# Optimization experiments

Hardware: AMD Instinct MI355X
Metric: run time of the kernel (lower is better)

## Reference

```python
import jax, jax.numpy as jnp
import numpy as np

B, T, Q, H = 128, 50, 1024, 256
MAX_STEP = 50
TEMP = 0.5
SUP_W, DIST_W, EMBED_W, LOSS_WEIGHT = 1.0, 0.01, 1.0, 1.0
BLUR, DIAMETER, REACH, SCALING, P = 0.005, 1.0, 500.0, 0.5, 2
NEG = -1e9


def _softmin(eps, C, h):
    # h: log-weights + potential/eps over the second axis of C
    return -eps * jax.nn.logsumexp(h[None, :] - C / eps, axis=1)


def _sqcost(u, v):
    sq = jnp.sum(u * u, -1)[:, None] + jnp.sum(v * v, -1)[None, :] - 2.0 * (u @ v.T)
    return 0.5 * jnp.maximum(sq, 0.0)  # geomloss p=2 cost: |x-y|^2 / 2


def sinkhorn_divergence(x, y):
    # geomloss SamplesLoss('sinkhorn', p=2, blur=0.005, diameter=1, reach=500),
    # tensorized, debiased, unbalanced, eps-scaling schedule.
    N, M = x.shape[0], y.shape[0]
    a_log = jnp.full((N,), -np.log(float(N)), dtype=x.dtype)
    b_log = jnp.full((M,), -np.log(float(M)), dtype=x.dtype)
    Cxy, Cyx = _sqcost(x, y), _sqcost(y, x)
    Cxx, Cyy = _sqcost(x, x), _sqcost(y, y)
    rho = REACH ** P
    eps_final = BLUR ** P
    eps_list = []
    e = DIAMETER ** P
    while e > eps_final:
        eps_list.append(e)
        e = e * (SCALING ** P)
    eps_list.append(eps_final)
    f_ab = jnp.zeros((N,), x.dtype)
    g_ab = jnp.zeros((M,), x.dtype)
    f_aa = jnp.zeros((N,), x.dtype)
    g_bb = jnp.zeros((M,), x.dtype)
    for eps in eps_list:  # static schedule (~9 steps)
        damp = 1.0 / (1.0 + eps / rho)
        ft = damp * _softmin(eps, Cxy, b_log + g_ab / eps)
        gt = damp * _softmin(eps, Cyx, a_log + f_ab / eps)
        faa = 0.5 * (f_aa + damp * _softmin(eps, Cxx, a_log + f_aa / eps))
        gbb = 0.5 * (g_bb + damp * _softmin(eps, Cyy, b_log + g_bb / eps))
        f_ab, g_ab, f_aa, g_bb = ft, gt, faa, gbb
    w = rho + eps_final / 2.0  # UnbalancedWeight
    a_w, b_w = jnp.exp(a_log), jnp.exp(b_log)
    return (jnp.sum(a_w * w * (jnp.exp(-f_aa / rho) - jnp.exp(-f_ab / rho)))
            + jnp.sum(b_w * w * (jnp.exp(-g_bb / rho) - jnp.exp(-g_ab / rho))))


def _forward(lc, lt, le, ltc, ltt, lte, ohs, oht, ods, odt, batch):
    p_c, p_t, p_e = lc / TEMP, lt / TEMP, le / TEMP
    q_c, q_t, q_e = ltc / TEMP, ltt / TEMP, lte / TEMP
    flat = lambda z: z.reshape(z.shape[0], -1)
    loss_kd = (sinkhorn_divergence(flat(p_c), flat(q_c))
               + sinkhorn_divergence(flat(p_t), flat(q_t))
               + sinkhorn_divergence(flat(p_e), flat(q_e)))
    S = MAX_STEP - 1
    delta = batch[:, :, :Q] + batch[:, :, Q:]  # [B,T,Q] question one-hots
    a = jnp.floor(((batch[:, :, :Q] - batch[:, :, Q:]).sum(-1) + 1.0) / 2.0)[:, 1:1 + S]  # [B,S] correctness
    dsh = delta[:, 1:1 + S]  # [B,S,Q]
    # diagonal of p[:S] @ delta[1:].T == per-step gather of next question's logit
    pc = jnp.einsum('bsq,bsq->bs', p_c[:, :S], dsh)
    pt = jnp.einsum('bsq,bsq->bs', p_t[:, :S], dsh)
    pe = jnp.einsum('bsq,bsq->bs', p_e[:, :S], dsh)
    idx = jnp.arange(S)
    last = jnp.max(jnp.where(pc > 0, idx[None, :], -1), axis=1)  # last i with pc[i] > 0
    L = jnp.where(last >= 0, last + 1, S)  # no break => keep full length
    mask = idx[None, :] < L[:, None]
    def ce(logits):
        m = jnp.where(mask, logits, NEG)
        lsm = m - jax.nn.logsumexp(m, axis=1, keepdims=True)
        return -jnp.sum(jnp.where(mask, a * lsm, 0.0))  # soft-target CE, summed over students
    loss_sup = ce(pt) + ce(pc) + ce(pe)
    embed = 0.5 * (jnp.sum((ohs - oht) ** 2) + jnp.sum((ods - odt) ** 2))
    total = LOSS_WEIGHT * (SUP_W * loss_sup + DIST_W * loss_kd + EMBED_W * embed)
    return total.reshape(1)


def setup_inputs():
    key = jax.random.key(0)
    ks = jax.random.split(key, 12)
    rn = lambda k, s: jax.random.normal(k, s, dtype=jnp.float32)
    qid = jax.random.randint(ks[10], (B, T), 0, Q)
    correct = jax.random.randint(ks[11], (B, T), 0, 2).astype(jnp.float32)
    oh = jax.nn.one_hot(qid, Q, dtype=jnp.float32)
    batch = jnp.concatenate([oh * correct[..., None], oh * (1.0 - correct)[..., None]], axis=-1)
    return {
        'logit_c': rn(ks[0], (B, T, Q)),
        'logit_t': rn(ks[1], (B, T, Q)),
        'logit_ensemble': rn(ks[2], (B, T, Q)),
        'logit_teacher_c': rn(ks[3], (B, T, Q)),
        'logit_teacher_t': rn(ks[4], (B, T, Q)),
        'logit_teacher_ensemble': rn(ks[5], (B, T, Q)),
        'out_h_student': rn(ks[6], (B, T, H)),
        'out_h_teacher': rn(ks[7], (B, T, H)),
        'out_d_student': rn(ks[8], (B, T, H)),
        'out_d_teacher': rn(ks[9], (B, T, H)),
        'batch': batch,
    }


def reference(logit_c, logit_t, logit_ensemble, logit_teacher_c, logit_teacher_t, logit_teacher_ensemble, out_h_student, out_h_teacher, out_d_student, out_d_teacher, batch):
    return _forward(logit_c, logit_t, logit_ensemble, logit_teacher_c, logit_teacher_t, logit_teacher_ensemble, out_h_student, out_h_teacher, out_d_student, out_d_teacher, batch)
```

## Files before the change

kernel.cpp:

```cpp
#include <hip/hip_runtime.h>

#define NB 128
#define T_DIM 50
#define Q_DIM 1024
#define H_DIM 256
#define S_DIM 49
#define K_DIM 51200
#define KCHUNKS 80
#define KC 640
#define BK 64
#define NSTAGE 10
#define GRAM_N (NB * NB)
#define LROWU 36
#define CPAD 132
#define PS_BLOCKS ((NB * S_DIM + 3) / 4)
#define EMB_BLOCKS 1600

typedef __attribute__((ext_vector_type(4))) float f32x4;
typedef __attribute__((ext_vector_type(8))) _Float16 half8v;
typedef __attribute__((ext_vector_type(4))) unsigned int uint4v;
typedef __attribute__((ext_vector_type(2))) unsigned int uint2v;
using pk2_t = decltype(__builtin_amdgcn_cvt_pkrtz(0.0f, 0.0f));

union PKU { pk2_t p; unsigned int u; };
union U4H8 { uint4v u; half8v h; };

__device__ inline unsigned short f2bf_rn(float x) {
  union { float f; unsigned int u; } v; v.f = x;
  unsigned int r = v.u + 0x7FFFu + ((v.u >> 16) & 1u);
  return (unsigned short)(r >> 16);
}
__device__ inline float bf2f(unsigned short b) {
  union { float f; unsigned int u; } v; v.u = ((unsigned int)b) << 16;
  return v.f;
}

__device__ __forceinline__ void issue_loads(
    const float* __restrict__ S, const float* __restrict__ Tm,
    size_t ro0, size_t ro1, int kpos, int kq,
    f32x4& p0, f32x4& p1, f32x4& p2, f32x4& p3) {
  const float* pS = S + kpos + kq * 4;
  const float* pT = Tm + kpos + kq * 4;
  p0 = *(const f32x4*)(pS + ro0);
  p1 = *(const f32x4*)(pS + ro1);
  p2 = *(const f32x4*)(pT + ro0);
  p3 = *(const f32x4*)(pT + ro1);
}

__device__ __forceinline__ void cvt_write(
    unsigned int* __restrict__ panA, unsigned int* __restrict__ panB,
    int r0, int kq,
    const f32x4& p0, const f32x4& p1, const f32x4& p2, const f32x4& p3) {
  PKU a, b; uint2v w;
  a.p = __builtin_amdgcn_cvt_pkrtz(p0[0], p0[1]);
  b.p = __builtin_amdgcn_cvt_pkrtz(p0[2], p0[3]);
  w.x = a.u; w.y = b.u;
  *(uint2v*)&panA[r0 * LROWU + kq * 2] = w;
  a.p = __builtin_amdgcn_cvt_pkrtz(p1[0], p1[1]);
  b.p = __builtin_amdgcn_cvt_pkrtz(p1[2], p1[3]);
  w.x = a.u; w.y = b.u;
  *(uint2v*)&panA[(r0 + 64) * LROWU + kq * 2] = w;
  a.p = __builtin_amdgcn_cvt_pkrtz(p2[0], p2[1]);
  b.p = __builtin_amdgcn_cvt_pkrtz(p2[2], p2[3]);
  w.x = a.u; w.y = b.u;
  *(uint2v*)&panB[r0 * LROWU + kq * 2] = w;
  a.p = __builtin_amdgcn_cvt_pkrtz(p3[0], p3[1]);
  b.p = __builtin_amdgcn_cvt_pkrtz(p3[2], p3[3]);
  w.x = a.u; w.y = b.u;
  *(uint2v*)&panB[(r0 + 64) * LROWU + kq * 2] = w;
}

__device__ __forceinline__ void compute_stage(
    const unsigned int* __restrict__ panA, const unsigned int* __restrict__ panB,
    int wrow, int wcol, int l15, int quad,
    f32x4 (&aXY)[2][2], f32x4 (&aXX)[2][2], f32x4 (&aYY)[2][2]) {
#pragma unroll
  for (int ks = 0; ks < 2; ks++) {
    const int kc = ks * 16 + quad * 4;
    half8v as_[2], bs_[2], at_[2], bt_[2];
#pragma unroll
    for (int t = 0; t < 2; t++) {
      U4H8 u;
      u.u = *(const uint4v*)&panA[(wrow * 32 + t * 16 + l15) * LROWU + kc]; as_[t] = u.h;
      u.u = *(const uint4v*)&panA[(wcol * 32 + t * 16 + l15) * LROWU + kc]; bs_[t] = u.h;
      u.u = *(const uint4v*)&panB[(wrow * 32 + t * 16 + l15) * LROWU + kc]; at_[t] = u.h;
      u.u = *(const uint4v*)&panB[(wcol * 32 + t * 16 + l15) * LROWU + kc]; bt_[t] = u.h;
    }
#pragma unroll
    for (int ti = 0; ti < 2; ti++)
#pragma unroll
      for (int tj = 0; tj < 2; tj++) {
        aXY[ti][tj] = __builtin_amdgcn_mfma_f32_16x16x32_f16(as_[ti], bt_[tj], aXY[ti][tj], 0, 0, 0);
        aXX[ti][tj] = __builtin_amdgcn_mfma_f32_16x16x32_f16(as_[ti], bs_[tj], aXX[ti][tj], 0, 0, 0);
        aYY[ti][tj] = __builtin_amdgcn_mfma_f32_16x16x32_f16(at_[ti], bt_[tj], aYY[ti][tj], 0, 0, 0);
      }
  }
}

__global__ __launch_bounds__(1024) void gram_fused_kernel(
    const float* __restrict__ s0, const float* __restrict__ s1, const float* __restrict__ s2,
    const float* __restrict__ t0, const float* __restrict__ t1, const float* __restrict__ t2,
    unsigned short* __restrict__ part) {
  __shared__ unsigned int pan[2][2][NB * LROWU];

  const int chunk = blockIdx.x;
  const int pair = blockIdx.y;
  const float* S  = (pair == 0) ? s0 : ((pair == 1) ? s1 : s2);
  const float* Tm = (pair == 0) ? t0 : ((pair == 1) ? t1 : t2);

  const int tid = threadIdx.x;
  const int wave = tid >> 6, lane = tid & 63;
  const int wrow = wave >> 2, wcol = wave & 3;
  const int l15 = lane & 15, quad = lane >> 4;

  f32x4 aXY[2][2], aXX[2][2], aYY[2][2];
#pragma unroll
  for (int i = 0; i < 2; i++)
#pragma unroll
    for (int j = 0; j < 2; j++) {
      aXY[i][j] = (f32x4){0.f, 0.f, 0.f, 0.f};
      aXX[i][j] = (f32x4){0.f, 0.f, 0.f, 0.f};
      aYY[i][j] = (f32x4){0.f, 0.f, 0.f, 0.f};
    }

  const int r0 = tid >> 4;
  const int kq = tid & 15;
  const size_t ro0 = (size_t)r0 * K_DIM;
  const size_t ro1 = (size_t)(r0 + 64) * K_DIM;
  const int kbase = chunk * KC;

  f32x4 A0, A1, A2, A3;
  f32x4 B0, B1, B2, B3;

  issue_loads(S, Tm, ro0, ro1, kbase, kq, A0, A1, A2, A3);
  issue_loads(S, Tm, ro0, ro1, kbase + BK, kq, B0, B1, B2, B3);
  cvt_write(&pan[0][0][0], &pan[0][1][0], r0, kq, A0, A1, A2, A3);
  __syncthreads();

  for (int s2 = 0; s2 < NSTAGE; s2 += 2) {
    if (s2 + 2 < NSTAGE)
      issue_loads(S, Tm, ro0, ro1, kbase + (s2 + 2) * BK, kq, A0, A1, A2, A3);
    compute_stage(&pan[0][0][0], &pan[0][1][0], wrow, wcol, l15, quad, aXY, aXX, aYY);
    cvt_write(&pan[1][0][0], &pan[1][1][0], r0, kq, B0, B1, B2, B3);
    __syncthreads();

    if (s2 + 3 < NSTAGE)
      issue_loads(S, Tm, ro0, ro1, kbase + (s2 + 3) * BK, kq, B0, B1, B2, B3);
    compute_stage(&pan[1][0][0], &pan[1][1][0], wrow, wcol, l15, quad, aXY, aXX, aYY);
    if (s2 + 2 < NSTAGE) {
      cvt_write(&pan[0][0][0], &pan[0][1][0], r0, kq, A0, A1, A2, A3);
      __syncthreads();
    }
  }

#pragma unroll
  for (int kind = 0; kind < 3; kind++) {
    unsigned short* out = part + ((size_t)(pair * 3 + kind) * KCHUNKS + chunk) * GRAM_N;
#pragma unroll
    for (int ti = 0; ti < 2; ti++)
#pragma unroll
      for (int tj = 0; tj < 2; tj++) {
        const f32x4 v = (kind == 0) ? aXY[ti][tj] : ((kind == 1) ? aXX[ti][tj] : aYY[ti][tj]);
        const int col = wcol * 32 + tj * 16 + l15;
#pragma unroll
        for (int r = 0; r < 4; r++) {
          const int row = wrow * 32 + ti * 16 + quad * 4 + r;
          out[(size_t)row * NB + col] = f2bf_rn(v[r]);
        }
      }
  }
}

__global__ __launch_bounds__(256) void gram_reduce_kernel(
    const unsigned short* __restrict__ part, float* __restrict__ gram) {
  const int idx = blockIdx.x * 256 + threadIdx.x;
  const int g = idx >> 14;
  const int cell = idx & (GRAM_N - 1);
  const unsigned short* p = part + (size_t)g * KCHUNKS * GRAM_N + cell;
  float s = 0.f;
#pragma unroll
  for (int c = 0; c < KCHUNKS; c++) s += bf2f(p[(size_t)c * GRAM_N]);
  gram[idx] = s;
}

__global__ __launch_bounds__(256, 1) void sinkhorn_part_kernel(
    const float* __restrict__ gram, float* __restrict__ kdpart) {
  const int pair = blockIdx.x, kind = blockIdx.y;
  const float* Gxy = gram + (size_t)(3 * pair + 0) * GRAM_N;
  const float* Gxx = gram + (size_t)(3 * pair + 1) * GRAM_N;
  const float* Gyy = gram + (size_t)(3 * pair + 2) * GRAM_N;

  __shared__ float CL[NB * CPAD];
  __shared__ f32x4 h4a[NB / 4];
  __shared__ f32x4 h4b[NB / 4];
  __shared__ float nx[NB], ny[NB];
  __shared__ float red[256];

  const int tid = threadIdx.x;
  if (tid < NB) {
    nx[tid] = Gxx[tid * (NB + 1)];
    ny[tid] = Gyy[tid * (NB + 1)];
    ((float*)h4a)[tid] = 0.f;
    ((float*)h4b)[tid] = 0.f;
  }
  __syncthreads();

  const float* G  = (kind == 0) ? Gxy : ((kind == 1) ? Gxx : Gyy);
  const float* rn = (kind == 2) ? ny : nx;
  const float* cn = (kind == 1) ? nx : ny;
  for (int idx = tid; idx < GRAM_N; idx += 256) {
    const int i = idx >> 7, j = idx & 127;
    CL[i * CPAD + j] = 2.0f * fmaxf(rn[i] + cn[j] - 2.0f * G[idx], 0.0f);
  }
  __syncthreads();

  const float rho = 250000.0f;
  const float AL = -4.852030263919617f;
  const float LOG2E = 1.4426950408889634f;
  const float LN2 = 0.6931471805599453f;
  const int grp = tid >> 7;
  const int i = tid & 127;
  const bool active = (kind == 0) || (grp == 0);
  const bool colread = (kind == 0) && (grp == 1);

  f32x4 crow[32];
  if (active) {
    if (colread) {
#pragma unroll
      for (int jj = 0; jj < 32; jj++) {
        f32x4 v;
        v[0] = CL[(4 * jj + 0) * CPAD + i];
        v[1] = CL[(4 * jj + 1) * CPAD + i];
        v[2] = CL[(4 * jj + 2) * CPAD + i];
        v[3] = CL[(4 * jj + 3) * CPAD + i];
        crow[jj] = v;
      }
    } else {
#pragma unroll
      for (int jj = 0; jj < 32; jj++)
        crow[jj] = *(const f32x4*)&CL[i * CPAD + 4 * jj];
    }
  }

  float eps = 1.0f;
  for (int it = 0; it < 9; it++) {
    if (it == 8) eps = 2.5e-5f;
    const float inv_eps = 1.0f / eps;
    const float damp = 1.0f / (1.0f + eps / rho);
    const float ebl = eps * AL;

    float newp = 0.f;
    if (active) {
      const f32x4* h = (kind == 0 && grp == 0) ? h4b : h4a;
      f32x4 m4 = (f32x4){-3.0e38f, -3.0e38f, -3.0e38f, -3.0e38f};
#pragma unroll
      for (int jj = 0; jj < 32; jj++) {
        const f32x4 u = h[jj] - crow[jj];
        m4[0] = fmaxf(m4[0], u[0]); m4[1] = fmaxf(m4[1], u[1]);
        m4[2] = fmaxf(m4[2], u[2]); m4[3] = fmaxf(m4[3], u[3]);
      }
      const float m = fmaxf(fmaxf(m4[0], m4[1]), fmaxf(m4[2], m4[3]));
      const float k = inv_eps * LOG2E;
      f32x4 s4 = (f32x4){0.f, 0.f, 0.f, 0.f};
#pragma unroll
      for (int jj = 0; jj < 32; jj++) {
        const f32x4 u = h[jj] - crow[jj];
        s4[0] += __builtin_exp2f((u[0] - m) * k);
        s4[1] += __builtin_exp2f((u[1] - m) * k);
        s4[2] += __builtin_exp2f((u[2] - m) * k);
        s4[3] += __builtin_exp2f((u[3] - m) * k);
      }
      const float Ssum = (s4[0] + s4[1]) + (s4[2] + s4[3]);
      const float sm = -(m + ebl + eps * (LN2 * __log2f(Ssum)));
      if (kind == 0) newp = damp * sm;
      else           newp = 0.5f * (((const float*)h4a)[i] + damp * sm);
    }
    __syncthreads();
    if (active) {
      if (grp == 0) ((float*)h4a)[i] = newp;
      else          ((float*)h4b)[i] = newp;
    }
    __syncthreads();
    eps *= 0.25f;
  }

  float v = 0.f;
  if (kind == 0) {
    v = (grp == 0) ? -__expf(-((const float*)h4a)[i] / rho)
                   : -__expf(-((const float*)h4b)[i] / rho);
  } else if (grp == 0) {
    v = __expf(-((const float*)h4a)[i] / rho);
  }
  red[tid] = v;
  __syncthreads();
  for (int st = 128; st > 0; st >>= 1) {
    if (tid < st) red[tid] += red[tid + st];
    __syncthreads();
  }
  if (tid == 0) kdpart[pair * 3 + kind] = red[0];
}

__global__ __launch_bounds__(256) void ps_embed_kernel(
    const float* __restrict__ lc, const float* __restrict__ lt, const float* __restrict__ le,
    const float* __restrict__ batch,
    const f32x4* __restrict__ hs, const f32x4* __restrict__ ht,
    const f32x4* __restrict__ ds, const f32x4* __restrict__ dt,
    float* __restrict__ pc, float* __restrict__ pt, float* __restrict__ pe,
    float* __restrict__ aarr, float* __restrict__ embPart) {
  const int bid = blockIdx.x;
  if (bid < PS_BLOCKS) {
    const int w = bid * 4 + (threadIdx.x >> 6);
    if (w >= NB * S_DIM) return;
    const int lane = threadIdx.x & 63;
    const int b = w / S_DIM, s = w - b * S_DIM;
    const float* brow = batch + ((size_t)b * T_DIM + (s + 1)) * (2 * Q_DIM);

    int qv = 0; float dsv = 0.f; bool found = false;
#pragma unroll
    for (int c = 0; c < 4; c++) {
      const int base = c * 256 + lane * 4;
      const f32x4 d0 = *(const f32x4*)(brow + base);
      const f32x4 d1 = *(const f32x4*)(brow + Q_DIM + base);
#pragma unroll
      for (int j = 0; j < 4; j++)
        if (d0[j] + d1[j] > 0.5f) { qv = base + j; dsv = d0[j] - d1[j]; found = true; }
    }
    const unsigned long long m = __ballot(found);
    const int src = (m != 0ull) ? (__ffsll((unsigned long long)m) - 1) : 0;
    qv = __shfl(qv, src, 64);
    dsv = __shfl(dsv, src, 64);
    if (lane == 0) {
      const size_t off = ((size_t)b * T_DIM + s) * Q_DIM + qv;
      pc[w] = 2.0f * lc[off];
      pt[w] = 2.0f * lt[off];
      pe[w] = 2.0f * le[off];
      aarr[w] = (m != 0ull && dsv > 0.0f) ? 1.0f : 0.0f;
    }
  } else {
    const int eb = bid - PS_BLOCKS;
    const int N4 = NB * T_DIM * H_DIM / 4;
    float sum = 0.f;
    for (int idx = eb * 256 + threadIdx.x; idx < N4; idx += EMB_BLOCKS * 256) {
      f32x4 a = hs[idx] - ht[idx];
      f32x4 b = ds[idx] - dt[idx];
      sum += a[0]*a[0] + a[1]*a[1] + a[2]*a[2] + a[3]*a[3]
           + b[0]*b[0] + b[1]*b[1] + b[2]*b[2] + b[3]*b[3];
    }
    for (int off = 32; off > 0; off >>= 1) sum += __shfl_down(sum, off, 64);
    __shared__ float wsum[4];
    const int lane = threadIdx.x & 63, wv = threadIdx.x >> 6;
    if (lane == 0) wsum[wv] = sum;
    __syncthreads();
    if (threadIdx.x == 0) embPart[eb] = wsum[0] + wsum[1] + wsum[2] + wsum[3];
  }
}

__global__ __launch_bounds__(128) void ce_final_kernel(
    const float* __restrict__ pc, const float* __restrict__ pt, const float* __restrict__ pe,
    const float* __restrict__ aarr, const float* __restrict__ kdpart,
    const float* __restrict__ embPart, float* __restrict__ out) {
  __shared__ float sx[4][NB][S_DIM];
  const int tid = threadIdx.x;
  for (int idx = tid; idx < NB * S_DIM; idx += 128) {
    const int b = idx / S_DIM, s = idx - b * S_DIM;
    sx[0][b][s] = pt[idx];
    sx[1][b][s] = pc[idx];
    sx[2][b][s] = pe[idx];
    sx[3][b][s] = aarr[idx];
  }
  float esum = 0.f;
  for (int i = tid; i < EMB_BLOCKS; i += 128) esum += embPart[i];
  __syncthreads();

  const int b = tid;
  int last = -1;
  for (int s = 0; s < S_DIM; s++)
    if (sx[1][b][s] > 0.0f) last = s;
  const int L = (last >= 0) ? (last + 1) : S_DIM;

  float loss = 0.f;
#pragma unroll
  for (int k = 0; k < 3; k++) {
    float m = -3.0e38f;
    for (int s = 0; s < L; s++) m = fmaxf(m, sx[k][b][s]);
    float sum = 0.f;
    for (int s = 0; s < L; s++) sum += __expf(sx[k][b][s] - m);
    const float lse = m + __logf(sum);
    float l = 0.f;
    for (int s = 0; s < L; s++) l += sx[3][b][s] * (sx[k][b][s] - lse);
    loss -= l;
  }

  __shared__ float red[128];
  __shared__ float rede[128];
  red[b] = loss;
  rede[b] = esum;
  __syncthreads();
  for (int st = 64; st > 0; st >>= 1) {
    if (b < st) { red[b] += red[b + st]; rede[b] += rede[b + st]; }
    __syncthreads();
  }
  if (b == 0) {
    float kd = 0.f;
    for (int k = 0; k < 9; k++) kd += kdpart[k];
    out[0] = red[0] + 0.01f * (250000.0000125f / 128.0f) * kd + 0.5f * rede[0];
  }
}

extern "C" void kernel_launch(void* const* d_in, const int* in_sizes, int n_in,
                              void* d_out, int out_size, void* d_ws, size_t ws_size,
                              hipStream_t stream) {
  const float* lc    = (const float*)d_in[0];
  const float* lt    = (const float*)d_in[1];
  const float* le    = (const float*)d_in[2];
  const float* ltc   = (const float*)d_in[3];
  const float* ltt   = (const float*)d_in[4];
  const float* lte   = (const float*)d_in[5];
  const float* ohs   = (const float*)d_in[6];
  const float* oht   = (const float*)d_in[7];
  const float* ods   = (const float*)d_in[8];
  const float* odt   = (const float*)d_in[9];
  const float* batch = (const float*)d_in[10];

  unsigned short* part = (unsigned short*)d_ws;
  float* gram = (float*)(part + (size_t)9 * KCHUNKS * GRAM_N);
  float* pcb  = gram + 9 * GRAM_N;
  float* ptb  = pcb + NB * S_DIM;
  float* peb  = ptb + NB * S_DIM;
  float* ab   = peb + NB * S_DIM;
  float* kdp  = ab + NB * S_DIM;
  float* embp = kdp + 9;

  ps_embed_kernel<<<PS_BLOCKS + EMB_BLOCKS, 256, 0, stream>>>(
      lc, lt, le, batch,
      (const f32x4*)ohs, (const f32x4*)oht, (const f32x4*)ods, (const f32x4*)odt,
      pcb, ptb, peb, ab, embp);

  gram_fused_kernel<<<dim3(KCHUNKS, 3), 1024, 0, stream>>>(lc, lt, le, ltc, ltt, lte, part);

  gram_reduce_kernel<<<(9 * GRAM_N) / 256, 256, 0, stream>>>(part, gram);

  sinkhorn_part_kernel<<<dim3(3, 3), 256, 0, stream>>>(gram, kdp);

  ce_final_kernel<<<1, 128, 0, stream>>>(pcb, ptb, peb, ab, kdp, embp, (float*)d_out);
}
```

Before: 323.4 us.

## Fuse gram, gather and embed kernels; fold CE into sinkhorn via last-block ticket

Merges the gram MFMA kernel with the per-step gather and embedding-MSE work into one 1024-thread launch, so the small memory-bound blocks run alongside the gram blocks instead of as a separate kernel. The final cross-entropy/combine kernel is folded into the sinkhorn kernel, where the last block to finish (found with an atomic ticket counter) computes the output. This removes two launches and their serialization gaps. In exchange the embed reduction moves from 1600 grid-stride blocks to 400 large blocks, the gram blocks' register-heavy launch bounds now apply to all blocks, and the code relies on a counter in workspace being reset correctly between calls.

Measured after the change: 319.7 us. No clear change (-1.1%).

```diff
diff --git a/kernel.cpp b/kernel.cpp
--- a/kernel.cpp
+++ b/kernel.cpp
@@ -13,8 +13,13 @@
 #define GRAM_N (NB * NB)
 #define LROWU 36
 #define CPAD 132
-#define PS_BLOCKS ((NB * S_DIM + 3) / 4)
-#define EMB_BLOCKS 1600
+
+#define GRAM_BLOCKS 240
+#define PS_BLOCKS 392
+#define EMB_BLOCKS 400
+#define PS_BASE GRAM_BLOCKS
+#define EMB_BASE (GRAM_BLOCKS + PS_BLOCKS)
+#define TOTAL_BLOCKS (EMB_BASE + EMB_BLOCKS)
 
 typedef __attribute__((ext_vector_type(4))) float f32x4;
 typedef __attribute__((ext_vector_type(8))) _Float16 half8v;
@@ -97,77 +102,133 @@
   }
 }
 
-__global__ __launch_bounds__(1024) void gram_fused_kernel(
+__global__ __launch_bounds__(1024) void mega_kernel(
     const float* __restrict__ s0, const float* __restrict__ s1, const float* __restrict__ s2,
     const float* __restrict__ t0, const float* __restrict__ t1, const float* __restrict__ t2,
-    unsigned short* __restrict__ part) {
+    const float* __restrict__ batch,
+    const f32x4* __restrict__ hs, const f32x4* __restrict__ ht,
+    const f32x4* __restrict__ ds, const f32x4* __restrict__ dt,
+    unsigned short* __restrict__ part,
+    float* __restrict__ pc, float* __restrict__ pt, float* __restrict__ pe,
+    float* __restrict__ aarr, float* __restrict__ embPart,
+    unsigned int* __restrict__ counter) {
   __shared__ unsigned int pan[2][2][NB * LROWU];
-
-  const int chunk = blockIdx.x;
-  const int pair = blockIdx.y;
-  const float* S  = (pair == 0) ? s0 : ((pair == 1) ? s1 : s2);
-  const float* Tm = (pair == 0) ? t0 : ((pair == 1) ? t1 : t2);
-
+  __shared__ float wsum[16];
+
+  const int bid = blockIdx.x;
   const int tid = threadIdx.x;
-  const int wave = tid >> 6, lane = tid & 63;
-  const int wrow = wave >> 2, wcol = wave & 3;
-  const int l15 = lane & 15, quad = lane >> 4;
-
-  f32x4 aXY[2][2], aXX[2][2], aYY[2][2];
-#pragma unroll
-  for (int i = 0; i < 2; i++)
-#pragma unroll
-    for (int j = 0; j < 2; j++) {
-      aXY[i][j] = (f32x4){0.f, 0.f, 0.f, 0.f};
-      aXX[i][j] = (f32x4){0.f, 0.f, 0.f, 0.f};
-      aYY[i][j] = (f32x4){0.f, 0.f, 0.f, 0.f};
-    }
-
-  const int r0 = tid >> 4;
-  const int kq = tid & 15;
-  const size_t ro0 = (size_t)r0 * K_DIM;
-  const size_t ro1 = (size_t)(r0 + 64) * K_DIM;
-  const int kbase = chunk * KC;
-
-  f32x4 A0, A1, A2, A3;
-  f32x4 B0, B1, B2, B3;
-
-  issue_loads(S, Tm, ro0, ro1, kbase, kq, A0, A1, A2, A3);
-  issue_loads(S, Tm, ro0, ro1, kbase + BK, kq, B0, B1, B2, B3);
-  cvt_write(&pan[0][0][0], &pan[0][1][0], r0, kq, A0, A1, A2, A3);
-  __syncthreads();
-
-  for (int s2 = 0; s2 < NSTAGE; s2 += 2) {
-    if (s2 + 2 < NSTAGE)
-      issue_loads(S, Tm, ro0, ro1, kbase + (s2 + 2) * BK, kq, A0, A1, A2, A3);
-    compute_stage(&pan[0][0][0], &pan[0][1][0], wrow, wcol, l15, quad, aXY, aXX, aYY);
-    cvt_write(&pan[1][0][0], &pan[1][1][0], r0, kq, B0, B1, B2, B3);
-    __syncthreads();
-
-    if (s2 + 3 < NSTAGE)
-      issue_loads(S, Tm, ro0, ro1, kbase + (s2 + 3) * BK, kq, B0, B1, B2, B3);
-    compute_stage(&pan[1][0][0], &pan[1][1][0], wrow, wcol, l15, quad, aXY, aXX, aYY);
-    if (s2 + 2 < NSTAGE) {
-      cvt_write(&pan[0][0][0], &pan[0][1][0], r0, kq, A0, A1, A2, A3);
+
+  if (bid == 0 && tid == 0) *counter = 0;
+
+  if (bid < GRAM_BLOCKS) {
+    const int chunk = bid % KCHUNKS;
+    const int pair = bid / KCHUNKS;
+    const float* S  = (pair == 0) ? s0 : ((pair == 1) ? s1 : s2);
+    const float* Tm = (pair == 0) ? t0 : ((pair == 1) ? t1 : t2);
+
+    const int wave = tid >> 6, lane = tid & 63;
+    const int wrow = wave >> 2, wcol = wave & 3;
+    const int l15 = lane & 15, quad = lane >> 4;
+
+    f32x4 aXY[2][2], aXX[2][2], aYY[2][2];
+#pragma unroll
+    for (int i = 0; i < 2; i++)
+#pragma unroll
+      for (int j = 0; j < 2; j++) {
+        aXY[i][j] = (f32x4){0.f, 0.f, 0.f, 0.f};
+        aXX[i][j] = (f32x4){0.f, 0.f, 0.f, 0.f};
+        aYY[i][j] = (f32x4){0.f, 0.f, 0.f, 0.f};
+      }
+
+    const int r0 = tid >> 4;
+    const int kq = tid & 15;
+    const size_t ro0 = (size_t)r0 * K_DIM;
+    const size_t ro1 = (size_t)(r0 + 64) * K_DIM;
+    const int kbase = chunk * KC;
+
+    f32x4 A0, A1, A2, A3, B0, B1, B2, B3;
+
+    issue_loads(S, Tm, ro0, ro1, kbase, kq, A0, A1, A2, A3);
+    issue_loads(S, Tm, ro0, ro1, kbase + BK, kq, B0, B1, B2, B3);
+    cvt_write(&pan[0][0][0], &pan[0][1][0], r0, kq, A0, A1, A2, A3);
+    __syncthreads();
+
+    for (int s2 = 0; s2 < NSTAGE; s2 += 2) {
+      if (s2 + 2 < NSTAGE)
+        issue_loads(S, Tm, ro0, ro1, kbase + (s2 + 2) * BK, kq, A0, A1, A2, A3);
+      compute_stage(&pan[0][0][0], &pan[0][1][0], wrow, wcol, l15, quad, aXY, aXX, aYY);
+      cvt_write(&pan[1][0][0], &pan[1][1][0], r0, kq, B0, B1, B2, B3);
       __syncthreads();
-    }
-  }
-
-#pragma unroll
-  for (int kind = 0; kind < 3; kind++) {
-    unsigned short* out = part + ((size_t)(pair * 3 + kind) * KCHUNKS + chunk) * GRAM_N;
-#pragma unroll
-    for (int ti = 0; ti < 2; ti++)
-#pragma unroll
-      for (int tj = 0; tj < 2; tj++) {
-        const f32x4 v = (kind == 0) ? aXY[ti][tj] : ((kind == 1) ? aXX[ti][tj] : aYY[ti][tj]);
-        const int col = wcol * 32 + tj * 16 + l15;
-#pragma unroll
-        for (int r = 0; r < 4; r++) {
-          const int row = wrow * 32 + ti * 16 + quad * 4 + r;
-          out[(size_t)row * NB + col] = f2bf_rn(v[r]);
+
+      if (s2 + 3 < NSTAGE)
+        issue_loads(S, Tm, ro0, ro1, kbase + (s2 + 3) * BK, kq, B0, B1, B2, B3);
+      compute_stage(&pan[1][0][0], &pan[1][1][0], wrow, wcol, l15, quad, aXY, aXX, aYY);
+      if (s2 + 2 < NSTAGE) {
+        cvt_write(&pan[0][0][0], &pan[0][1][0], r0, kq, A0, A1, A2, A3);
+        __syncthreads();
+      }
+    }
+
+#pragma unroll
+    for (int kind = 0; kind < 3; kind++) {
+      unsigned short* out = part + ((size_t)(pair * 3 + kind) * KCHUNKS + chunk) * GRAM_N;
+#pragma unroll
+      for (int ti = 0; ti < 2; ti++)
+#pragma unroll
+        for (int tj = 0; tj < 2; tj++) {
+          const f32x4 v = (kind == 0) ? aXY[ti][tj] : ((kind == 1) ? aXX[ti][tj] : aYY[ti][tj]);
+          const int col = wcol * 32 + tj * 16 + l15;
+#pragma unroll
+          for (int r = 0; r < 4; r++) {
+            const int row = wrow * 32 + ti * 16 + quad * 4 + r;
+            out[(size_t)row * NB + col] = f2bf_rn(v[r]);
+          }
         }
-      }
+    }
+  } else if (bid < EMB_BASE) {
+    const int w = (bid - PS_BASE) * 16 + (tid >> 6);
+    const int lane = tid & 63;
+    const int b = w / S_DIM, s = w - b * S_DIM;
+    const float* brow = batch + ((size_t)b * T_DIM + (s + 1)) * (2 * Q_DIM);
+
+    int qv = 0; float dsv = 0.f; bool found = false;
+#pragma unroll
+    for (int c = 0; c < 4; c++) {
+      const int base = c * 256 + lane * 4;
+      const f32x4 d0 = *(const f32x4*)(brow + base);
+      const f32x4 d1 = *(const f32x4*)(brow + Q_DIM + base);
+#pragma unroll
+      for (int j = 0; j < 4; j++)
+        if (d0[j] + d1[j] > 0.5f) { qv = base + j; dsv = d0[j] - d1[j]; found = true; }
+    }
+    const unsigned long long m = __ballot(found);
+    const int src = (m != 0ull) ? (__ffsll((unsigned long long)m) - 1) : 0;
+    qv = __shfl(qv, src, 64);
+    dsv = __shfl(dsv, src, 64);
+    if (lane == 0) {
+      const size_t off = ((size_t)b * T_DIM + s) * Q_DIM + qv;
+      pc[w] = 2.0f * s0[off];
+      pt[w] = 2.0f * s1[off];
+      pe[w] = 2.0f * s2[off];
+      aarr[w] = (m != 0ull && dsv > 0.0f) ? 1.0f : 0.0f;
+    }
+  } else {
+    const int eb = bid - EMB_BASE;
+    const int idx = eb * 1024 + tid;
+    const f32x4 a = hs[idx] - ht[idx];
+    const f32x4 b = ds[idx] - dt[idx];
+    float sum = a[0]*a[0] + a[1]*a[1] + a[2]*a[2] + a[3]*a[3]
+              + b[0]*b[0] + b[1]*b[1] + b[2]*b[2] + b[3]*b[3];
+    for (int off = 32; off > 0; off >>= 1) sum += __shfl_down(sum, off, 64);
+    const int lane = tid & 63, wv = tid >> 6;
+    if (lane == 0) wsum[wv] = sum;
+    __syncthreads();
+    if (tid == 0) {
+      float t = 0.f;
+#pragma unroll
+      for (int i = 0; i < 16; i++) t += wsum[i];
+      embPart[eb] = t;
+    }
   }
 }
 
@@ -183,34 +244,48 @@
   gram[idx] = s;
 }
 
-__global__ __launch_bounds__(256, 1) void sinkhorn_part_kernel(
-    const float* __restrict__ gram, float* __restrict__ kdpart) {
+union SHU {
+  struct {
+    float CL[NB * CPAD];
+    float h[2][NB];
+    float nx[NB], ny[NB];
+    float red[256];
+  } s;
+  struct {
+    float sx[4][NB][S_DIM];
+    float red[256], rede[256];
+  } c;
+};
+
+__global__ __launch_bounds__(256, 1) void sinkhorn_ce_kernel(
+    const float* __restrict__ gram, float* __restrict__ kdpart,
+    const float* __restrict__ pcb, const float* __restrict__ ptb,
+    const float* __restrict__ peb, const float* __restrict__ ab,
+    const float* __restrict__ embPart, unsigned int* __restrict__ counter,
+    float* __restrict__ outp) {
+  __shared__ SHU sh;
+  __shared__ int ticket;
+
   const int pair = blockIdx.x, kind = blockIdx.y;
   const float* Gxy = gram + (size_t)(3 * pair + 0) * GRAM_N;
   const float* Gxx = gram + (size_t)(3 * pair + 1) * GRAM_N;
   const float* Gyy = gram + (size_t)(3 * pair + 2) * GRAM_N;
 
-  __shared__ float CL[NB * CPAD];
-  __shared__ f32x4 h4a[NB / 4];
-  __shared__ f32x4 h4b[NB / 4];
-  __shared__ float nx[NB], ny[NB];
-  __shared__ float red[256];
-
   const int tid = threadIdx.x;
   if (tid < NB) {
-    nx[tid] = Gxx[tid * (NB + 1)];
-    ny[tid] = Gyy[tid * (NB + 1)];
-    ((float*)h4a)[tid] = 0.f;
-    ((float*)h4b)[tid] = 0.f;
+    sh.s.nx[tid] = Gxx[tid * (NB + 1)];
+    sh.s.ny[tid] = Gyy[tid * (NB + 1)];
+    sh.s.h[0][tid] = 0.f;
+    sh.s.h[1][tid] = 0.f;
   }
   __syncthreads();
 
   const float* G  = (kind == 0) ? Gxy : ((kind == 1) ? Gxx : Gyy);
-  const float* rn = (kind == 2) ? ny : nx;
-  const float* cn = (kind == 1) ? nx : ny;
+  const float* rn = (kind == 2) ? sh.s.ny : sh.s.nx;
+  const float* cn = (kind == 1) ? sh.s.nx : sh.s.ny;
   for (int idx = tid; idx < GRAM_N; idx += 256) {
     const int i = idx >> 7, j = idx & 127;
-    CL[i * CPAD + j] = 2.0f * fmaxf(rn[i] + cn[j] - 2.0f * G[idx], 0.0f);
+    sh.s.CL[i * CPAD + j] = 2.0f * fmaxf(rn[i] + cn[j] - 2.0f * G[idx], 0.0f);
   }
   __syncthreads();
 
@@ -229,16 +304,16 @@
 #pragma unroll
       for (int jj = 0; jj < 32; jj++) {
         f32x4 v;
-        v[0] = CL[(4 * jj + 0) * CPAD + i];
-        v[1] = CL[(4 * jj + 1) * CPAD + i];
-        v[2] = CL[(4 * jj + 2) * CPAD + i];
-        v[3] = CL[(4 * jj + 3) * CPAD + i];
+        v[0] = sh.s.CL[(4 * jj + 0) * CPAD + i];
+        v[1] = sh.s.CL[(4 * jj + 1) * CPAD + i];
+        v[2] = sh.s.CL[(4 * jj + 2) * CPAD + i];
+        v[3] = sh.s.CL[(4 * jj + 3) * CPAD + i];
         crow[jj] = v;
       }
     } else {
 #pragma unroll
       for (int jj = 0; jj < 32; jj++)
-        crow[jj] = *(const f32x4*)&CL[i * CPAD + 4 * jj];
+        crow[jj] = *(const f32x4*)&sh.s.CL[i * CPAD + 4 * jj];
     }
   }
 
@@ -251,7 +326,8 @@
 
     float newp = 0.f;
     if (active) {
-      const f32x4* h = (kind == 0 && grp == 0) ? h4b : h4a;
+      const int hsel = (kind == 0 && grp == 0) ? 1 : 0;
+      const f32x4* h = (const f32x4*)sh.s.h[hsel];
       f32x4 m4 = (f32x4){-3.0e38f, -3.0e38f, -3.0e38f, -3.0e38f};
 #pragma unroll
       for (int jj = 0; jj < 32; jj++) {
@@ -273,137 +349,78 @@
       const float Ssum = (s4[0] + s4[1]) + (s4[2] + s4[3]);
       const float sm = -(m + ebl + eps * (LN2 * __log2f(Ssum)));
       if (kind == 0) newp = damp * sm;
-      else           newp = 0.5f * (((const float*)h4a)[i] + damp * sm);
-    }
-    __syncthreads();
-    if (active) {
-      if (grp == 0) ((float*)h4a)[i] = newp;
-      else          ((float*)h4b)[i] = newp;
-    }
+      else           newp = 0.5f * (sh.s.h[0][i] + damp * sm);
+    }
+    __syncthreads();
+    if (active) sh.s.h[grp][i] = newp;
     __syncthreads();
     eps *= 0.25f;
   }
 
   float v = 0.f;
   if (kind == 0) {
-    v = (grp == 0) ? -__expf(-((const float*)h4a)[i] / rho)
-                   : -__expf(-((const float*)h4b)[i] / rho);
+    v = (grp == 0) ? -__expf(-sh.s.h[0][i] / rho)
+                   : -__expf(-sh.s.h[1][i] / rho);
   } else if (grp == 0) {
-    v = __expf(-((const float*)h4a)[i] / rho);
-  }
-  red[tid] = v;
+    v = __expf(-sh.s.h[0][i] / rho);
+  }
+  sh.s.red[tid] = v;
   __syncthreads();
   for (int st = 128; st > 0; st >>= 1) {
-    if (tid < st) red[tid] += red[tid + st];
-    __syncthreads();
-  }
-  if (tid == 0) kdpart[pair * 3 + kind] = red[0];
-}
-
-__global__ __launch_bounds__(256) void ps_embed_kernel(
-    const float* __restrict__ lc, const float* __restrict__ lt, const float* __restrict__ le,
-    const float* __restrict__ batch,
-    const f32x4* __restrict__ hs, const f32x4* __restrict__ ht,
-    const f32x4* __restrict__ ds, const f32x4* __restrict__ dt,
-    float* __restrict__ pc, float* __restrict__ pt, float* __restrict__ pe,
-    float* __restrict__ aarr, float* __restrict__ embPart) {
-  const int bid = blockIdx.x;
-  if (bid < PS_BLOCKS) {
-    const int w = bid * 4 + (threadIdx.x >> 6);
-    if (w >= NB * S_DIM) return;
-    const int lane = threadIdx.x & 63;
-    const int b = w / S_DIM, s = w - b * S_DIM;
-    const float* brow = batch + ((size_t)b * T_DIM + (s + 1)) * (2 * Q_DIM);
-
-    int qv = 0; float dsv = 0.f; bool found = false;
-#pragma unroll
-    for (int c = 0; c < 4; c++) {
-      const int base = c * 256 + lane * 4;
-      const f32x4 d0 = *(const f32x4*)(brow + base);
-      const f32x4 d1 = *(const f32x4*)(brow + Q_DIM + base);
-#pragma unroll
-      for (int j = 0; j < 4; j++)
-        if (d0[j] + d1[j] > 0.5f) { qv = base + j; dsv = d0[j] - d1[j]; found = true; }
-    }
-    const unsigned long long m = __ballot(found);
-    const int src = (m != 0ull) ? (__ffsll((unsigned long long)m) - 1) : 0;
-    qv = __shfl(qv, src, 64);
-    dsv = __shfl(dsv, src, 64);
-    if (lane == 0) {
-      const size_t off = ((size_t)b * T_DIM + s) * Q_DIM + qv;
-      pc[w] = 2.0f * lc[off];
-      pt[w] = 2.0f * lt[off];
-      pe[w] = 2.0f * le[off];
-      aarr[w] = (m != 0ull && dsv > 0.0f) ? 1.0f : 0.0f;
-    }
-  } else {
-    const int eb = bid - PS_BLOCKS;
-    const int N4 = NB * T_DIM * H_DIM / 4;
-    float sum = 0.f;
-    for (int idx = eb * 256 + threadIdx.x; idx < N4; idx += EMB_BLOCKS * 256) {
-      f32x4 a = hs[idx] - ht[idx];
-      f32x4 b = ds[idx] - dt[idx];
-      sum += a[0]*a[0] + a[1]*a[1] + a[2]*a[2] + a[3]*a[3]
-           + b[0]*b[0] + b[1]*b[1] + b[2]*b[2] + b[3]*b[3];
-    }
-    for (int off = 32; off > 0; off >>= 1) sum += __shfl_down(sum, off, 64);
-    __shared__ float wsum[4];
-    const int lane = threadIdx.x & 63, wv = threadIdx.x >> 6;
-    if (lane == 0) wsum[wv] = sum;
-    __syncthreads();
-    if (threadIdx.x == 0) embPart[eb] = wsum[0] + wsum[1] + wsum[2] + wsum[3];
-  }
-}
-
-__global__ __launch_bounds__(128) void ce_final_kernel(
-    const float* __restrict__ pc, const float* __restrict__ pt, const float* __restrict__ pe,
-    const float* __restrict__ aarr, const float* __restrict__ kdpart,
-    const float* __restrict__ embPart, float* __restrict__ out) {
-  __shared__ float sx[4][NB][S_DIM];
-  const int tid = threadIdx.x;
-  for (int idx = tid; idx < NB * S_DIM; idx += 128) {
+    if (tid < st) sh.s.red[tid] += sh.s.red[tid + st];
+    __syncthreads();
+  }
+  if (tid == 0) kdpart[pair * 3 + kind] = sh.s.red[0];
+
+  __threadfence();
+  __syncthreads();
+  if (tid == 0) ticket = (int)atomicAdd(counter, 1u);
+  __syncthreads();
+  if (ticket != 8) return;
+  __threadfence();
+
+  for (int idx = tid; idx < NB * S_DIM; idx += 256) {
     const int b = idx / S_DIM, s = idx - b * S_DIM;
-    sx[0][b][s] = pt[idx];
-    sx[1][b][s] = pc[idx];
-    sx[2][b][s] = pe[idx];
-    sx[3][b][s] = aarr[idx];
+    sh.c.sx[0][b][s] = ptb[idx];
+    sh.c.sx[1][b][s] = pcb[idx];
+    sh.c.sx[2][b][s] = peb[idx];
+    sh.c.sx[3][b][s] = ab[idx];
   }
   float esum = 0.f;
-  for (int i = tid; i < EMB_BLOCKS; i += 128) esum += embPart[i];
-  __syncthreads();
-
-  const int b = tid;
-  int last = -1;
-  for (int s = 0; s < S_DIM; s++)
-    if (sx[1][b][s] > 0.0f) last = s;
-  const int L = (last >= 0) ? (last + 1) : S_DIM;
+  for (int j = tid; j < EMB_BLOCKS; j += 256) esum += embPart[j];
+  __syncthreads();
 
   float loss = 0.f;
-#pragma unroll
-  for (int k = 0; k < 3; k++) {
-    float m = -3.0e38f;
-    for (int s = 0; s < L; s++) m = fmaxf(m, sx[k][b][s]);
-    float sum = 0.f;
-    for (int s = 0; s < L; s++) sum += __expf(sx[k][b][s] - m);
-    const float lse = m + __logf(sum);
-    float l = 0.f;
-    for (int s = 0; s < L; s++) l += sx[3][b][s] * (sx[k][b][s] - lse);
-    loss -= l;
-  }
-
-  __shared__ float red[128];
-  __shared__ float rede[128];
-  red[b] = loss;
-  rede[b] = esum;
-  __syncthreads();
-  for (int st = 64; st > 0; st >>= 1) {
-    if (b < st) { red[b] += red[b + st]; rede[b] += rede[b + st]; }
-    __syncthreads();
-  }
-  if (b == 0) {
+  if (tid < NB) {
+    const int b = tid;
+    int last = -1;
+    for (int s = 0; s < S_DIM; s++)
+      if (sh.c.sx[1][b][s] > 0.0f) last = s;
+    const int L = (last >= 0) ? (last + 1) : S_DIM;
+#pragma unroll
+    for (int k = 0; k < 3; k++) {
+      float m = -3.0e38f;
+      for (int s = 0; s < L; s++) m = fmaxf(m, sh.c.sx[k][b][s]);
+      float sum = 0.f;
+      for (int s = 0; s < L; s++) sum += __expf(sh.c.sx[k][b][s] - m);
+      const float lse = m + __logf(sum);
+      float l = 0.f;
+      for (int s = 0; s < L; s++) l += sh.c.sx[3][b][s] * (sh.c.sx[k][b][s] - lse);
+      loss -= l;
+    }
+  }
+  sh.c.red[tid] = loss;
+  sh.c.rede[tid] = esum;
+  __syncthreads();
+  for (int st = 128; st > 0; st >>= 1) {
+    if (tid < st) { sh.c.red[tid] += sh.c.red[tid + st]; sh.c.rede[tid] += sh.c.rede[tid + st]; }
+    __syncthreads();
+  }
+  if (tid == 0) {
     float kd = 0.f;
     for (int k = 0; k < 9; k++) kd += kdpart[k];
-    out[0] = red[0] + 0.01f * (250000.0000125f / 128.0f) * kd + 0.5f * rede[0];
+    outp[0] = sh.c.red[0] + 0.01f * (250000.0000125f / 128.0f) * kd + 0.5f * sh.c.rede[0];
+    *counter = 0;
   }
 }
 
@@ -430,17 +447,15 @@
   float* ab   = peb + NB * S_DIM;
   float* kdp  = ab + NB * S_DIM;
   float* embp = kdp + 9;
-
-  ps_embed_kernel<<<PS_BLOCKS + EMB_BLOCKS, 256, 0, stream>>>(
-      lc, lt, le, batch,
+  unsigned int* counter = (unsigned int*)(embp + EMB_BLOCKS);
+
+  mega_kernel<<<TOTAL_BLOCKS, 1024, 0, stream>>>(
+      lc, lt, le, ltc, ltt, lte, batch,
       (const f32x4*)ohs, (const f32x4*)oht, (const f32x4*)ods, (const f32x4*)odt,
-      pcb, ptb, peb, ab, embp);
-
-  gram_fused_kernel<<<dim3(KCHUNKS, 3), 1024, 0, stream>>>(lc, lt, le, ltc, ltt, lte, part);
+      part, pcb, ptb, peb, ab, embp, counter);
 
   gram_reduce_kernel<<<(9 * GRAM_N) / 256, 256, 0, stream>>>(part, gram);
 
-  sinkhorn_part_kernel<<<dim3(3, 3), 256, 0, stream>>>(gram, kdp);
-
-  ce_final_kernel<<<1, 128, 0, stream>>>(pcb, ptb, peb, ab, kdp, embp, (float*)d_out);
-}
+  sinkhorn_ce_kernel<<<dim3(3, 3), 256, 0, stream>>>(
+      gram, kdp, pcb, ptb, peb, ab, embp, counter, (float*)d_out);
+}
```
